# Optimization experiments

Hardware: AMD Instinct MI355X
Metric: run time of the kernel (lower is better)

The kernel has to match this reference:

```python
import jax, jax.numpy as jnp
import numpy as np

N, F, H, C, E, L = 100000, 512, 64, 40, 1600000, 6


def setup_inputs() -> dict:
    key = jax.random.key(0)
    ks = jax.random.split(key, 2 * L + 4)
    x = jax.random.normal(ks[0], (N, F), dtype=jnp.float32)
    edge_index = jax.random.randint(ks[1], (2, E), 0, N, dtype=jnp.int32)
    inp = {"x": x, "edge_index": edge_index}
    in_dims = [F + H * i for i in range(L)]  # 512, 576, ..., 832 (dense concat)
    for i in range(L):
        inp[f"W{i}"] = jax.random.normal(ks[2 + i], (in_dims[i], H), dtype=jnp.float32) / np.sqrt(in_dims[i]).astype(np.float32)
        inp[f"b{i}"] = jnp.zeros((H,), dtype=jnp.float32)
    jk_dim = in_dims[-1] + H  # 896 = num_features + 6*H
    inp["Wlin"] = jax.random.normal(ks[2 + L], (jk_dim, C), dtype=jnp.float32) / np.sqrt(jk_dim).astype(np.float32)
    inp["blin"] = jnp.zeros((C,), dtype=jnp.float32)
    return inp


def _gcn_norm(edge_index, num_nodes, dtype):
    # Add self loops, compute symmetric normalization deg^-1/2 * deg^-1/2
    loop = jnp.arange(num_nodes, dtype=edge_index.dtype)
    row = jnp.concatenate([edge_index[0], loop])  # source
    col = jnp.concatenate([edge_index[1], loop])  # target
    deg = jax.ops.segment_sum(jnp.ones_like(col, dtype=dtype), col, num_segments=num_nodes)
    dinv = jnp.where(deg > 0, jax.lax.rsqrt(jnp.maximum(deg, 1.0)), 0.0)
    norm = dinv[row] * dinv[col]  # [E + N]
    return row, col, norm


def reference(x, edge_index, W0, b0, W1, b1, W2, b2, W3, b3, W4, b4, W5, b5, Wlin, blin):
    Ws = [W0, W1, W2, W3, W4, W5]
    bs = [b0, b1, b2, b3, b4, b5]
    n = x.shape[0]
    row, col, norm = _gcn_norm(edge_index, n, x.dtype)

    xs = [x]
    for W, b in zip(Ws, bs):
        inp = jnp.concatenate(xs, axis=1)          # dense (DenseNet-style) concat
        lin = inp @ W                               # [n, H] transform before propagate
        msg = lin[row] * norm[:, None]              # gather + edge weight
        agg = jax.ops.segment_sum(msg, col, num_segments=n)  # scatter-add aggregate
        h = jax.nn.relu(agg + b)                    # GCNConv bias, then ReLU (dropout = eval mode)
        xs.append(h)

    hcat = jnp.concatenate(xs, axis=1)              # JumpingKnowledge('cat')
    logits = hcat @ Wlin + blin
    return jax.nn.log_softmax(logits, axis=1)
```

## Files before the change

kernel.cpp:

```cpp
#include <hip/hip_runtime.h>
#include <hip/hip_bf16.h>

#define HH 64
#define XDIM 896
#define FF 512
#define LL 6
#define CC 40
#define CBSZ 512
#define SLACK 10240
#define NSEG 13

typedef __bf16 bf16x8 __attribute__((ext_vector_type(8)));
typedef float f32x4 __attribute__((ext_vector_type(4)));

__device__ __forceinline__ unsigned short f2bf(float f){
  union{float f; unsigned int u;} v; v.f=f; unsigned int u=v.u;
  return (unsigned short)((u + 0x7fffu + ((u>>16)&1u))>>16);
}
__device__ __forceinline__ float bf2f(unsigned short u){
  union{unsigned int u; float f;} v; v.u = ((unsigned int)u)<<16; return v.f;
}
__device__ __forceinline__ float u2f(unsigned u){
  union{unsigned u; float f;} v; v.u=u; return v.f;
}

#define GLD16(gsrc, ldsdst) \
  __builtin_amdgcn_global_load_lds((const __attribute__((address_space(1))) unsigned int*)(gsrc), \
                                   (__attribute__((address_space(3))) unsigned int*)(ldsdst), 16, 0, 0)

struct PrepP {
  const float* x; const int* ei;
  unsigned short* X; unsigned short* lin;
  int* bcur; unsigned* tmp;
  const float* W[NSEG]; unsigned short* dst[NSEG];
  int nt[NSEG], nc[NSEG], tst[NSEG], tbs[NSEG], kbase[NSEG];
  int off[NSEG+1];
  int N, E, CH, NB, WB;
};

__global__ void __launch_bounds__(256) k_prep(PrepP P){
  __shared__ int hist[256];
  __shared__ int run[256];
  int t=threadIdx.x, b=blockIdx.x;
  if (b < 256){
    int E=P.E;
    int lo=b*P.CH, hi=lo+P.CH; if (hi>E) hi=E;
    for (int i=t;i<P.NB;i+=256) hist[i]=0;
    __syncthreads();
    for (int i=lo+t;i<hi;i+=256) atomicAdd(&hist[P.ei[E+i]>>9], 1);
    __syncthreads();
    for (int i=t;i<P.NB;i+=256) run[i]=i*SLACK+atomicAdd(&P.bcur[i], hist[i]);
    __syncthreads();
    for (int i=lo+t;i<hi;i+=256){
      int r=P.ei[i], c=P.ei[E+i];
      int pos=atomicAdd(&run[c>>9],1);
      P.tmp[pos]=((unsigned)r<<9)|(unsigned)(c&(CBSZ-1));
    }
  } else if (b < 256+P.WB){
    int idx=(b-256)*256+t;
    if (idx < P.off[NSEG]){
      int seg=0;
      while (idx>=P.off[seg+1]) ++seg;
      int li=idx-P.off[seg];
      int j=li&7, ln=(li>>3)&63, rem2=li>>9;
      int ntile=P.nt[seg], ncols=P.nc[seg];
      int nt_=rem2%ntile, kb=rem2/ntile;
      int k=P.kbase[seg]+kb*32+(ln>>4)*8+j;
      int c=nt_*16+(ln&15);
      float v=(c<ncols)? P.W[seg][(size_t)k*ncols+c] : 0.f;
      int di = ((kb*P.tst[seg] + P.tbs[seg] + nt_)*64 + ln)*8 + j;
      P.dst[seg][di]=f2bf(v);
    }
  } else {
    int i=(b-256-P.WB)*256+t;
    if (i<32) ((unsigned*)(P.lin+(size_t)P.N*64))[i]=0u;
    int total=P.N*(FF/4);
    if (i<total){
      int row=i/(FF/4), c4=(i%(FF/4))*4;
      float4 v=*(const float4*)(P.x+(size_t)row*FF+c4);
      ushort4 o; o.x=f2bf(v.x); o.y=f2bf(v.y); o.z=f2bf(v.z); o.w=f2bf(v.w);
      *(ushort4*)(P.X+(size_t)row*XDIM+c4)=o;
    }
  }
}

__global__ void __launch_bounds__(1024) k_build(const unsigned* __restrict__ tmp,
                                                const int* __restrict__ bcur,
                                                int* __restrict__ offsS, int* __restrict__ offsE,
                                                float* __restrict__ dinv,
                                                int* __restrict__ esrc, int N){
  __shared__ int cnt[CBSZ];
  __shared__ int run[CBSZ];
  int t=threadIdx.x, b=blockIdx.x;
  int n0=b*CBSZ;
  int nloc=N-n0; if (nloc>CBSZ) nloc=CBSZ;
  int wbase=b*SLACK;
  int wend=wbase + bcur[b];
  if (t<CBSZ) cnt[t]=0;
  __syncthreads();
  for (int i=wbase+t; i<wend; i+=1024) atomicAdd(&cnt[tmp[i]&(CBSZ-1u)],1);
  __syncthreads();
  int v = (t<CBSZ)? cnt[t] : 0;
  if (t<CBSZ) run[t]=v;
  __syncthreads();
  for (int o=1;o<CBSZ;o<<=1){
    int xx = (t<CBSZ && t>=o)? run[t-o] : 0;
    __syncthreads();
    if (t<CBSZ) run[t]+=xx;
    __syncthreads();
  }
  if (t<nloc){
    int s = wbase + (run[t]-v);
    offsS[n0+t]=s;
    offsE[n0+t]=s+v;
    dinv[n0+t]=rsqrtf((float)(v+1));
    run[t]=s;
  }
  __syncthreads();
  for (int i=wbase+t; i<wend; i+=1024){
    unsigned vv=tmp[i];
    int pos=atomicAdd(&run[vv&(CBSZ-1u)],1);
    esrc[pos]=(int)(vv>>9);
  }
}

struct GBP {
  const unsigned short* X; const unsigned short* WfBig;
  const float* dinv;
  unsigned short* pl[6];
  float* pF;
  int N;
};

__global__ void __launch_bounds__(256) k_gbig(GBP P){
  __shared__ unsigned short Abuf[2][128*32];
  int t=threadIdx.x, lane=t&63, wv=t>>6;
  int bid = blockIdx.x;
  int cg = bid & 3;
  long rb = (long)(bid>>2)*128;
  int tb = cg*7;
  int arow=lane&15, kgrp=lane>>4;

  int srow0 = wv*32 + (lane>>2);
  int srow1 = srow0 + 16;
  int scb   = 16*((lane&3) ^ (srow0&3));
  long gr0 = rb + srow0; if (gr0 > (long)P.N-1) gr0 = P.N-1;
  long gr1 = rb + srow1; if (gr1 > (long)P.N-1) gr1 = P.N-1;
  const char* gs0 = (const char*)P.X + gr0*(XDIM*2) + scb;
  const char* gs1 = (const char*)P.X + gr1*(XDIM*2) + scb;

  f32x4 acc0[7], acc1[7];
  #pragma unroll
  for (int i=0;i<7;i++){ f32x4 z={0.f,0.f,0.f,0.f}; acc0[i]=z; acc1[i]=z; }

  GLD16(gs0, &Abuf[0][(wv*2+0)*512]);
  GLD16(gs1, &Abuf[0][(wv*2+1)*512]);
  __syncthreads();

  int kofs = 16*(kgrp ^ (arow&3));
  for (int kb=0;kb<16;++kb){
    int cur = kb&1;
    if (kb<15){
      GLD16(gs0 + (kb+1)*64, &Abuf[cur^1][(wv*2+0)*512]);
      GLD16(gs1 + (kb+1)*64, &Abuf[cur^1][(wv*2+1)*512]);
    }
    const unsigned short* bp = P.WfBig + ((size_t)kb*28 + tb)*512 + lane*8;
    bf16x8 bv[7];
    #pragma unroll
    for (int tt=0;tt<7;++tt) bv[tt]=*(const bf16x8*)(bp + (size_t)tt*512);
    int lr0 = wv*32 + arow;
    bf16x8 a0 = *(const bf16x8*)((const char*)&Abuf[cur][0] + lr0*64 + kofs);
    bf16x8 a1 = *(const bf16x8*)((const char*)&Abuf[cur][0] + (lr0+16)*64 + kofs);
    #pragma unroll
    for (int tt=0;tt<7;++tt){
      acc0[tt]=__builtin_amdgcn_mfma_f32_16x16x32_bf16(a0,bv[tt],acc0[tt],0,0,0);
      acc1[tt]=__builtin_amdgcn_mfma_f32_16x16x32_bf16(a1,bv[tt],acc1[tt],0,0,0);
    }
    __syncthreads();
  }

  long row0 = rb + wv*32;
  #pragma unroll
  for (int tt=0;tt<7;++tt){
    int tg = tb+tt;
    if (tg >= 27) continue;
    #pragma unroll
    for (int j=0;j<4;++j){
      long rr=row0+kgrp*4+j;
      long rr1=rr+16;
      if (tg<24){
        int li=tg>>2, tloc=tg&3;
        if (rr<P.N){
          float s = (li==0) ? P.dinv[rr] : 1.f;
          P.pl[li][(size_t)rr*64 + tloc*16 + arow] = f2bf(acc0[tt][j]*s);
        }
        if (rr1<P.N){
          float s = (li==0) ? P.dinv[rr1] : 1.f;
          P.pl[li][(size_t)rr1*64 + tloc*16 + arow] = f2bf(acc1[tt][j]*s);
        }
      } else {
        int c=(tg-24)*16+arow;
        if (c<CC){
          if (rr<P.N)  P.pF[(size_t)rr*CC+c]=acc0[tt][j];
          if (rr1<P.N) P.pF[(size_t)rr1*CC+c]=acc1[tt][j];
        }
      }
    }
  }
}

__global__ void __launch_bounds__(256) k_gemmH(const unsigned short* __restrict__ X,
                                               const unsigned short* __restrict__ WfH,
                                               const unsigned short* __restrict__ part,
                                               const float* __restrict__ dinv,
                                               unsigned short* __restrict__ lin,
                                               int N, int nkb2){
  int lane = threadIdx.x & 63, wid = threadIdx.x >> 6;
  long row0 = (long)blockIdx.x*128 + wid*32;
  int arow = lane & 15, kgrp = lane >> 4;
  long r0 = row0 + arow;      if (r0 > (long)N-1) r0 = N-1;
  long r1 = row0 + 16 + arow; if (r1 > (long)N-1) r1 = N-1;
  const unsigned short* ap0 = X + (size_t)r0*XDIM + FF + kgrp*8;
  const unsigned short* ap1 = X + (size_t)r1*XDIM + FF + kgrp*8;
  const unsigned short* bptr = WfH + lane*8;
  f32x4 acc00={0.f,0.f,0.f,0.f}, acc01=acc00, acc02=acc00, acc03=acc00;
  f32x4 acc10=acc00, acc11=acc00, acc12=acc00, acc13=acc00;
  for (int kb=0; kb<nkb2; ++kb){
    bf16x8 a0 = *(const bf16x8*)(ap0 + (size_t)kb*32);
    bf16x8 a1 = *(const bf16x8*)(ap1 + (size_t)kb*32);
    const unsigned short* bp = bptr + (size_t)kb*2048;
    bf16x8 b0=*(const bf16x8*)bp, b1=*(const bf16x8*)(bp+512),
           b2=*(const bf16x8*)(bp+1024), b3=*(const bf16x8*)(bp+1536);
    acc00=__builtin_amdgcn_mfma_f32_16x16x32_bf16(a0,b0,acc00,0,0,0);
    acc10=__builtin_amdgcn_mfma_f32_16x16x32_bf16(a1,b0,acc10,0,0,0);
    acc01=__builtin_amdgcn_mfma_f32_16x16x32_bf16(a0,b1,acc01,0,0,0);
    acc11=__builtin_amdgcn_mfma_f32_16x16x32_bf16(a1,b1,acc11,0,0,0);
    acc02=__builtin_amdgcn_mfma_f32_16x16x32_bf16(a0,b2,acc02,0,0,0);
    acc12=__builtin_amdgcn_mfma_f32_16x16x32_bf16(a1,b2,acc12,0,0,0);
    acc03=__builtin_amdgcn_mfma_f32_16x16x32_bf16(a0,b3,acc03,0,0,0);
    acc13=__builtin_amdgcn_mfma_f32_16x16x32_bf16(a1,b3,acc13,0,0,0);
  }
  for (int j=0;j<4;++j){
    long rr = row0 + kgrp*4 + j;
    if (rr < N){
      float dv = dinv[rr];
      const unsigned short* pp = part + (size_t)rr*64 + arow;
      unsigned short* lp = lin + (size_t)rr*64 + arow;
      lp[0]  = f2bf((acc00[j]+bf2f(pp[0]))*dv);
      lp[16] = f2bf((acc01[j]+bf2f(pp[16]))*dv);
      lp[32] = f2bf((acc02[j]+bf2f(pp[32]))*dv);
      lp[48] = f2bf((acc03[j]+bf2f(pp[48]))*dv);
    }
    long rr1 = rr + 16;
    if (rr1 < N){
      float dv = dinv[rr1];
      const unsigned short* pp = part + (size_t)rr1*64 + arow;
      unsigned short* lp = lin + (size_t)rr1*64 + arow;
      lp[0]  = f2bf((acc10[j]+bf2f(pp[0]))*dv);
      lp[16] = f2bf((acc11[j]+bf2f(pp[16]))*dv);
      lp[32] = f2bf((acc12[j]+bf2f(pp[32]))*dv);
      lp[48] = f2bf((acc13[j]+bf2f(pp[48]))*dv);
    }
  }
}

__global__ void __launch_bounds__(256) k_agg(const unsigned short* __restrict__ lin,
                                             const int* __restrict__ offsS,
                                             const int* __restrict__ offsE,
                                             const int* __restrict__ esrc,
                                             const float* __restrict__ dinv,
                                             const float* __restrict__ bias,
                                             unsigned short* __restrict__ X,
                                             int colbase, int N){
  int lane = threadIdx.x & 63, wid = threadIdx.x >> 6;
  int n = blockIdx.x*4 + wid;
  if (n >= N) return;
  int sub = lane >> 4;
  int fq  = lane & 15;
  const unsigned short* lq = lin + fq*4;
  float a0=0.f, a1=0.f, a2=0.f, a3=0.f;
  int s = offsS[n], e = offsE[n];
  int base = s;
  for (; base + 32 <= e; base += 32){
    #pragma unroll
    for (int k=0;k<8;++k){
      int sx = esrc[base + 4*k + sub];
      uint2 v = *(const uint2*)(lq + (size_t)sx*64);
      a0 += u2f(v.x<<16); a1 += u2f(v.x&0xffff0000u);
      a2 += u2f(v.y<<16); a3 += u2f(v.y&0xffff0000u);
    }
  }
  if (base < e){
    int rem = e - base;
    if (rem > 16){
      #pragma unroll
      for (int k=0;k<8;++k){
        int idx = 4*k + sub;
        int sx = esrc[base + idx];
        sx = (idx < rem) ? sx : (int)N;
        uint2 v = *(const uint2*)(lq + (size_t)sx*64);
        a0 += u2f(v.x<<16); a1 += u2f(v.x&0xffff0000u);
        a2 += u2f(v.y<<16); a3 += u2f(v.y&0xffff0000u);
      }
    } else {
      #pragma unroll
      for (int k=0;k<4;++k){
        int idx = 4*k + sub;
        int sx = esrc[base + idx];
        sx = (idx < rem) ? sx : (int)N;
        uint2 v = *(const uint2*)(lq + (size_t)sx*64);
        a0 += u2f(v.x<<16); a1 += u2f(v.x&0xffff0000u);
        a2 += u2f(v.y<<16); a3 += u2f(v.y&0xffff0000u);
      }
    }
  }
  a0 += __shfl_xor(a0,16,64); a0 += __shfl_xor(a0,32,64);
  a1 += __shfl_xor(a1,16,64); a1 += __shfl_xor(a1,32,64);
  a2 += __shfl_xor(a2,16,64); a2 += __shfl_xor(a2,32,64);
  a3 += __shfl_xor(a3,16,64); a3 += __shfl_xor(a3,32,64);
  uint2 vs = *(const uint2*)(lq + (size_t)n*64);
  a0 += u2f(vs.x<<16); a1 += u2f(vs.x&0xffff0000u);
  a2 += u2f(vs.y<<16); a3 += u2f(vs.y&0xffff0000u);
  float dv = dinv[n];
  float4 b4 = *(const float4*)(bias + fq*4);
  float h0 = fmaxf(a0*dv + b4.x, 0.f);
  float h1 = fmaxf(a1*dv + b4.y, 0.f);
  float h2 = fmaxf(a2*dv + b4.z, 0.f);
  float h3 = fmaxf(a3*dv + b4.w, 0.f);
  if (sub == 0){
    ushort4 o; o.x=f2bf(h0); o.y=f2bf(h1); o.z=f2bf(h2); o.w=f2bf(h3);
    *(ushort4*)(X + (size_t)n*XDIM + colbase + fq*4) = o;
  }
}

__global__ void __launch_bounds__(256) k_final(const unsigned short* __restrict__ X,
                                               const unsigned short* __restrict__ Wf,
                                               const float* __restrict__ pF,
                                               const float* __restrict__ blin,
                                               float* __restrict__ out, int N){
  int lane=threadIdx.x&63, wid=threadIdx.x>>6;
  long row0=(long)blockIdx.x*64 + wid*16;
  int c0=lane&15, g=lane>>4;
  long r=row0+c0; if (r > (long)N-1) r = N-1;
  const unsigned short* aptr = X + (size_t)r*XDIM + FF + g*8;
  const unsigned short* bptr = Wf + lane*8;
  f32x4 acc0={0.f,0.f,0.f,0.f}, acc1=acc0, acc2=acc0;
  const int nkb = (XDIM-FF)/32;
  for (int kb=0;kb<nkb;++kb){
    bf16x8 a=*(const bf16x8*)(aptr+(size_t)kb*32);
    const unsigned short* bp = bptr + (size_t)kb*1536;
    bf16x8 b0=*(const bf16x8*)bp, b1=*(const bf16x8*)(bp+512), b2=*(const bf16x8*)(bp+1024);
    acc0=__builtin_amdgcn_mfma_f32_16x16x32_bf16(a,b0,acc0,0,0,0);
    acc1=__builtin_amdgcn_mfma_f32_16x16x32_bf16(a,b1,acc1,0,0,0);
    acc2=__builtin_amdgcn_mfma_f32_16x16x32_bf16(a,b2,acc2,0,0,0);
  }
  float bl0 = blin[c0], bl1 = blin[16+c0];
  bool v2ok = (c0 < 8);
  float bl2 = v2ok ? blin[32+c0] : 0.f;
  for (int j=0;j<4;++j){
    long rr = row0 + g*4 + j;
    long rrc = rr < N ? rr : (long)N-1;
    const float* pp = pF + (size_t)rrc*CC;
    float v0 = acc0[j]+bl0+pp[c0], v1 = acc1[j]+bl1+pp[16+c0];
    float v2 = v2ok ? (acc2[j]+bl2+pp[32+c0]) : -1e30f;
    float m = fmaxf(fmaxf(v0,v1),v2);
    m = fmaxf(m, __shfl_xor(m,1,64));
    m = fmaxf(m, __shfl_xor(m,2,64));
    m = fmaxf(m, __shfl_xor(m,4,64));
    m = fmaxf(m, __shfl_xor(m,8,64));
    float sEx = expf(v0-m)+expf(v1-m)+(v2ok?expf(v2-m):0.f);
    sEx += __shfl_xor(sEx,1,64);
    sEx += __shfl_xor(sEx,2,64);
    sEx += __shfl_xor(sEx,4,64);
    sEx += __shfl_xor(sEx,8,64);
    float lse = m + logf(sEx);
    if (rr < N){
      out[(size_t)rr*CC + c0]      = v0 - lse;
      out[(size_t)rr*CC + 16 + c0] = v1 - lse;
      if (v2ok) out[(size_t)rr*CC + 32 + c0] = v2 - lse;
    }
  }
}

extern "C" void kernel_launch(void* const* d_in, const int* in_sizes, int n_in,
                              void* d_out, int out_size, void* d_ws, size_t ws_size,
                              hipStream_t stream){
  const float* x = (const float*)d_in[0];
  const int* ei = (const int*)d_in[1];
  const float* Wl[LL]; const float* bl[LL];
  for (int i=0;i<LL;i++){ Wl[i]=(const float*)d_in[2+2*i]; bl[i]=(const float*)d_in[3+2*i]; }
  const float* Wlin = (const float*)d_in[2+2*LL];
  const float* blin = (const float*)d_in[3+2*LL];
  float* out = (float*)d_out;
  const int N = in_sizes[0]/FF;
  const int E = in_sizes[1]/2;
  const int NB = (N+CBSZ-1)/CBSZ;

  char* p = (char*)d_ws;
  auto alloc = [&](size_t bb)->char*{ char* r=p; p += (bb+255)&~(size_t)255; return r; };
  unsigned short* X   = (unsigned short*)alloc((size_t)N*XDIM*2);
  unsigned short* lin = (unsigned short*)alloc((size_t)(N+1)*64*2);
  unsigned* tmp = (unsigned*)lin;
  unsigned short* WfBig  = (unsigned short*)alloc((size_t)16*28*512*2);
  unsigned short* WfH[LL];
  for (int i=1;i<LL;i++) WfH[i]=(unsigned short*)alloc((size_t)(2*i)*4*512*2);
  unsigned short* WfLinH = (unsigned short*)alloc((size_t)12*3*512*2);
  unsigned short* part[LL];
  for (int i=1;i<LL;i++) part[i]=(unsigned short*)alloc((size_t)N*64*2);
  float* pF    = (float*)alloc((size_t)N*CC*4);
  float* dinv  = (float*)alloc((size_t)N*4);
  int* offsS   = (int*)alloc((size_t)N*4);
  int* offsE   = (int*)alloc((size_t)N*4);
  int* bcur    = (int*)alloc((size_t)NB*4);
  int* esrc    = (int*)alloc(((size_t)NB*SLACK+64)*4);

  PrepP P;
  P.x=x; P.ei=ei; P.X=X; P.lin=lin; P.bcur=bcur; P.tmp=tmp;
  int off=0, sg=0;
  for (int i=0;i<LL;i++){
    P.W[sg]=Wl[i]; P.dst[sg]=WfBig; P.nt[sg]=4; P.nc[sg]=HH;
    P.tst[sg]=28; P.tbs[sg]=4*i; P.kbase[sg]=0;
    P.off[sg]=off; off += 16*4*512; ++sg;
  }
  P.W[sg]=Wlin; P.dst[sg]=WfBig; P.nt[sg]=3; P.nc[sg]=CC;
  P.tst[sg]=28; P.tbs[sg]=24; P.kbase[sg]=0;
  P.off[sg]=off; off += 16*3*512; ++sg;
  for (int i=1;i<LL;i++){
    P.W[sg]=Wl[i]; P.dst[sg]=WfH[i]; P.nt[sg]=4; P.nc[sg]=HH;
    P.tst[sg]=4; P.tbs[sg]=0; P.kbase[sg]=FF;
    P.off[sg]=off; off += (2*i)*4*512; ++sg;
  }
  P.W[sg]=Wlin; P.dst[sg]=WfLinH; P.nt[sg]=3; P.nc[sg]=CC;
  P.tst[sg]=3; P.tbs[sg]=0; P.kbase[sg]=FF;
  P.off[sg]=off; off += 12*3*512; ++sg;
  P.off[sg]=off;
  P.N=N; P.E=E; P.CH=(E+255)/256; P.NB=NB; P.WB=(off+255)/256;
  int XB=(N*(FF/4)+255)/256;

  hipMemsetAsync(bcur, 0, (size_t)NB*4, stream);
  k_prep <<<256 + P.WB + XB, 256, 0, stream>>>(P);
  k_build<<<NB, 1024, 0, stream>>>(tmp, bcur, offsS, offsE, dinv, esrc, N);

  GBP G;
  G.X=X; G.WfBig=WfBig; G.dinv=dinv;
  G.pl[0]=lin;
  for (int i=1;i<LL;i++) G.pl[i]=part[i];
  G.pF=pF; G.N=N;
  int rbks = (N+127)/128;
  k_gbig<<<rbks*4, 256, 0, stream>>>(G);

  int gb = (N+127)/128;
  int ab = (N+3)/4;
  for (int i=0;i<LL;i++){
    if (i>0) k_gemmH<<<gb,256,0,stream>>>(X, WfH[i], part[i], dinv, lin, N, 2*i);
    k_agg<<<ab,256,0,stream>>>(lin, offsS, offsE, esrc, dinv, bl[i], X, FF+HH*i, N);
  }
  k_final<<<(N+63)/64,256,0,stream>>>(X, WfLinH, pF, blin, out, N);
}
```

Measured before the change: 594.7 us.

## Split lin into four 16-column planes and aggregate one plane per block

```diff
diff --git a/kernel.cpp b/kernel.cpp
--- a/kernel.cpp
+++ b/kernel.cpp
@@ -73,7 +73,6 @@
     }
   } else {
     int i=(b-256-P.WB)*256+t;
-    if (i<32) ((unsigned*)(P.lin+(size_t)P.N*64))[i]=0u;
     int total=P.N*(FF/4);
     if (i<total){
       int row=i/(FF/4), c4=(i%(FF/4))*4;
@@ -136,6 +135,10 @@
   __shared__ unsigned short Abuf[2][128*32];
   int t=threadIdx.x, lane=t&63, wv=t>>6;
   int bid = blockIdx.x;
+  if (bid==0 && t<32){
+    int c=t>>3, d=t&7;
+    ((unsigned*)(P.pl[0] + ((size_t)c*(P.N+1) + P.N)*16))[d] = 0u;
+  }
   int cg = bid & 3;
   long rb = (long)(bid>>2)*128;
   int tb = cg*7;
@@ -190,13 +193,12 @@
       long rr1=rr+16;
       if (tg<24){
         int li=tg>>2, tloc=tg&3;
-        if (rr<P.N){
-          float s = (li==0) ? P.dinv[rr] : 1.f;
-          P.pl[li][(size_t)rr*64 + tloc*16 + arow] = f2bf(acc0[tt][j]*s);
-        }
-        if (rr1<P.N){
-          float s = (li==0) ? P.dinv[rr1] : 1.f;
-          P.pl[li][(size_t)rr1*64 + tloc*16 + arow] = f2bf(acc1[tt][j]*s);
+        if (li==0){
+          if (rr<P.N)  P.pl[0][((size_t)tloc*(P.N+1)+rr )*16 + arow] = f2bf(acc0[tt][j]*P.dinv[rr]);
+          if (rr1<P.N) P.pl[0][((size_t)tloc*(P.N+1)+rr1)*16 + arow] = f2bf(acc1[tt][j]*P.dinv[rr1]);
+        } else {
+          if (rr<P.N)  P.pl[li][(size_t)rr *64 + tloc*16 + arow] = f2bf(acc0[tt][j]);
+          if (rr1<P.N) P.pl[li][(size_t)rr1*64 + tloc*16 + arow] = f2bf(acc1[tt][j]);
         }
       } else {
         int c=(tg-24)*16+arow;
@@ -245,91 +247,83 @@
     if (rr < N){
       float dv = dinv[rr];
       const unsigned short* pp = part + (size_t)rr*64 + arow;
-      unsigned short* lp = lin + (size_t)rr*64 + arow;
-      lp[0]  = f2bf((acc00[j]+bf2f(pp[0]))*dv);
-      lp[16] = f2bf((acc01[j]+bf2f(pp[16]))*dv);
-      lp[32] = f2bf((acc02[j]+bf2f(pp[32]))*dv);
-      lp[48] = f2bf((acc03[j]+bf2f(pp[48]))*dv);
+      lin[((size_t)0*(N+1)+rr)*16 + arow] = f2bf((acc00[j]+bf2f(pp[0]))*dv);
+      lin[((size_t)1*(N+1)+rr)*16 + arow] = f2bf((acc01[j]+bf2f(pp[16]))*dv);
+      lin[((size_t)2*(N+1)+rr)*16 + arow] = f2bf((acc02[j]+bf2f(pp[32]))*dv);
+      lin[((size_t)3*(N+1)+rr)*16 + arow] = f2bf((acc03[j]+bf2f(pp[48]))*dv);
     }
     long rr1 = rr + 16;
     if (rr1 < N){
       float dv = dinv[rr1];
       const unsigned short* pp = part + (size_t)rr1*64 + arow;
-      unsigned short* lp = lin + (size_t)rr1*64 + arow;
-      lp[0]  = f2bf((acc10[j]+bf2f(pp[0]))*dv);
-      lp[16] = f2bf((acc11[j]+bf2f(pp[16]))*dv);
-      lp[32] = f2bf((acc12[j]+bf2f(pp[32]))*dv);
-      lp[48] = f2bf((acc13[j]+bf2f(pp[48]))*dv);
-    }
-  }
-}
-
-__global__ void __launch_bounds__(256) k_agg(const unsigned short* __restrict__ lin,
+      lin[((size_t)0*(N+1)+rr1)*16 + arow] = f2bf((acc10[j]+bf2f(pp[0]))*dv);
+      lin[((size_t)1*(N+1)+rr1)*16 + arow] = f2bf((acc11[j]+bf2f(pp[16]))*dv);
+      lin[((size_t)2*(N+1)+rr1)*16 + arow] = f2bf((acc12[j]+bf2f(pp[32]))*dv);
+      lin[((size_t)3*(N+1)+rr1)*16 + arow] = f2bf((acc13[j]+bf2f(pp[48]))*dv);
+    }
+  }
+}
+
+__global__ void __launch_bounds__(256) k_agg(const unsigned short* __restrict__ lin4,
                                              const int* __restrict__ offsS,
                                              const int* __restrict__ offsE,
                                              const int* __restrict__ esrc,
                                              const float* __restrict__ dinv,
                                              const float* __restrict__ bias,
                                              unsigned short* __restrict__ X,
-                                             int colbase, int N){
+                                             int colbase, int N, int nb4){
   int lane = threadIdx.x & 63, wid = threadIdx.x >> 6;
-  int n = blockIdx.x*4 + wid;
+  int chunk = blockIdx.x / nb4;
+  int nbid  = blockIdx.x - chunk*nb4;
+  int n = nbid*4 + wid;
   if (n >= N) return;
-  int sub = lane >> 4;
-  int fq  = lane & 15;
-  const unsigned short* lq = lin + fq*4;
-  float a0=0.f, a1=0.f, a2=0.f, a3=0.f;
+  int sub = lane >> 2;
+  int fj  = lane & 3;
+  const unsigned short* lq = lin4 + (size_t)chunk*(N+1)*16 + fj*4;
+  float a0=0.f,a1=0.f,a2=0.f,a3=0.f;
   int s = offsS[n], e = offsE[n];
   int base = s;
   for (; base + 32 <= e; base += 32){
-    #pragma unroll
-    for (int k=0;k<8;++k){
-      int sx = esrc[base + 4*k + sub];
-      uint2 v = *(const uint2*)(lq + (size_t)sx*64);
-      a0 += u2f(v.x<<16); a1 += u2f(v.x&0xffff0000u);
-      a2 += u2f(v.y<<16); a3 += u2f(v.y&0xffff0000u);
-    }
+    int sx0 = esrc[base + sub];
+    int sx1 = esrc[base + 16 + sub];
+    uint2 v0 = *(const uint2*)(lq + (size_t)sx0*16);
+    uint2 v1 = *(const uint2*)(lq + (size_t)sx1*16);
+    a0 += u2f(v0.x<<16); a1 += u2f(v0.x&0xffff0000u);
+    a2 += u2f(v0.y<<16); a3 += u2f(v0.y&0xffff0000u);
+    a0 += u2f(v1.x<<16); a1 += u2f(v1.x&0xffff0000u);
+    a2 += u2f(v1.y<<16); a3 += u2f(v1.y&0xffff0000u);
   }
   if (base < e){
     int rem = e - base;
+    int sx0 = esrc[base + sub];
+    sx0 = (sub < rem) ? sx0 : (int)N;
+    uint2 v0 = *(const uint2*)(lq + (size_t)sx0*16);
+    a0 += u2f(v0.x<<16); a1 += u2f(v0.x&0xffff0000u);
+    a2 += u2f(v0.y<<16); a3 += u2f(v0.y&0xffff0000u);
     if (rem > 16){
-      #pragma unroll
-      for (int k=0;k<8;++k){
-        int idx = 4*k + sub;
-        int sx = esrc[base + idx];
-        sx = (idx < rem) ? sx : (int)N;
-        uint2 v = *(const uint2*)(lq + (size_t)sx*64);
-        a0 += u2f(v.x<<16); a1 += u2f(v.x&0xffff0000u);
-        a2 += u2f(v.y<<16); a3 += u2f(v.y&0xffff0000u);
-      }
-    } else {
-      #pragma unroll
-      for (int k=0;k<4;++k){
-        int idx = 4*k + sub;
-        int sx = esrc[base + idx];
-        sx = (idx < rem) ? sx : (int)N;
-        uint2 v = *(const uint2*)(lq + (size_t)sx*64);
-        a0 += u2f(v.x<<16); a1 += u2f(v.x&0xffff0000u);
-        a2 += u2f(v.y<<16); a3 += u2f(v.y&0xffff0000u);
-      }
-    }
-  }
-  a0 += __shfl_xor(a0,16,64); a0 += __shfl_xor(a0,32,64);
-  a1 += __shfl_xor(a1,16,64); a1 += __shfl_xor(a1,32,64);
-  a2 += __shfl_xor(a2,16,64); a2 += __shfl_xor(a2,32,64);
-  a3 += __shfl_xor(a3,16,64); a3 += __shfl_xor(a3,32,64);
-  uint2 vs = *(const uint2*)(lq + (size_t)n*64);
+      int sx1 = esrc[base + 16 + sub];
+      sx1 = (16 + sub < rem) ? sx1 : (int)N;
+      uint2 v1 = *(const uint2*)(lq + (size_t)sx1*16);
+      a0 += u2f(v1.x<<16); a1 += u2f(v1.x&0xffff0000u);
+      a2 += u2f(v1.y<<16); a3 += u2f(v1.y&0xffff0000u);
+    }
+  }
+  a0 += __shfl_xor(a0,4,64); a0 += __shfl_xor(a0,8,64); a0 += __shfl_xor(a0,16,64); a0 += __shfl_xor(a0,32,64);
+  a1 += __shfl_xor(a1,4,64); a1 += __shfl_xor(a1,8,64); a1 += __shfl_xor(a1,16,64); a1 += __shfl_xor(a1,32,64);
+  a2 += __shfl_xor(a2,4,64); a2 += __shfl_xor(a2,8,64); a2 += __shfl_xor(a2,16,64); a2 += __shfl_xor(a2,32,64);
+  a3 += __shfl_xor(a3,4,64); a3 += __shfl_xor(a3,8,64); a3 += __shfl_xor(a3,16,64); a3 += __shfl_xor(a3,32,64);
+  uint2 vs = *(const uint2*)(lq + (size_t)n*16);
   a0 += u2f(vs.x<<16); a1 += u2f(vs.x&0xffff0000u);
   a2 += u2f(vs.y<<16); a3 += u2f(vs.y&0xffff0000u);
   float dv = dinv[n];
-  float4 b4 = *(const float4*)(bias + fq*4);
+  float4 b4 = *(const float4*)(bias + chunk*16 + fj*4);
   float h0 = fmaxf(a0*dv + b4.x, 0.f);
   float h1 = fmaxf(a1*dv + b4.y, 0.f);
   float h2 = fmaxf(a2*dv + b4.z, 0.f);
   float h3 = fmaxf(a3*dv + b4.w, 0.f);
   if (sub == 0){
     ushort4 o; o.x=f2bf(h0); o.y=f2bf(h1); o.z=f2bf(h2); o.w=f2bf(h3);
-    *(ushort4*)(X + (size_t)n*XDIM + colbase + fq*4) = o;
+    *(ushort4*)(X + (size_t)n*XDIM + colbase + chunk*16 + fj*4) = o;
   }
 }
 
@@ -399,7 +393,7 @@
   char* p = (char*)d_ws;
   auto alloc = [&](size_t bb)->char*{ char* r=p; p += (bb+255)&~(size_t)255; return r; };
   unsigned short* X   = (unsigned short*)alloc((size_t)N*XDIM*2);
-  unsigned short* lin = (unsigned short*)alloc((size_t)(N+1)*64*2);
+  unsigned short* lin = (unsigned short*)alloc((size_t)4*(N+1)*16*2);
   unsigned* tmp = (unsigned*)lin;
   unsigned short* WfBig  = (unsigned short*)alloc((size_t)16*28*512*2);
   unsigned short* WfH[LL];
@@ -453,7 +447,7 @@
   int ab = (N+3)/4;
   for (int i=0;i<LL;i++){
     if (i>0) k_gemmH<<<gb,256,0,stream>>>(X, WfH[i], part[i], dinv, lin, N, 2*i);
-    k_agg<<<ab,256,0,stream>>>(lin, offsS, offsE, esrc, dinv, bl[i], X, FF+HH*i, N);
+    k_agg<<<4*ab,256,0,stream>>>(lin, offsS, offsE, esrc, dinv, bl[i], X, FF+HH*i, N, ab);
   }
   k_final<<<(N+63)/64,256,0,stream>>>(X, WfLinH, pF, blin, out, N);
 }
```

Result: slower. 1.089 ms (+83.0%).

## Remap k_gbig blocks to 32 rows with waves splitting output column tiles

Applied to the files above, without the earlier changes.

```diff
diff --git a/kernel.cpp b/kernel.cpp
--- a/kernel.cpp
+++ b/kernel.cpp
@@ -133,44 +133,37 @@
 };
 
 __global__ void __launch_bounds__(256) k_gbig(GBP P){
-  __shared__ unsigned short Abuf[2][128*32];
+  __shared__ unsigned short Abuf[2][1024];
   int t=threadIdx.x, lane=t&63, wv=t>>6;
-  int bid = blockIdx.x;
-  int cg = bid & 3;
-  long rb = (long)(bid>>2)*128;
-  int tb = cg*7;
+  int tb = wv*7;
+  long rb = (long)blockIdx.x*32;
   int arow=lane&15, kgrp=lane>>4;
 
-  int srow0 = wv*32 + (lane>>2);
-  int srow1 = srow0 + 16;
-  int scb   = 16*((lane&3) ^ (srow0&3));
-  long gr0 = rb + srow0; if (gr0 > (long)P.N-1) gr0 = P.N-1;
-  long gr1 = rb + srow1; if (gr1 > (long)P.N-1) gr1 = P.N-1;
-  const char* gs0 = (const char*)P.X + gr0*(XDIM*2) + scb;
-  const char* gs1 = (const char*)P.X + gr1*(XDIM*2) + scb;
+  const char* gs = nullptr;
+  if (wv < 2){
+    int srow = wv*16 + (lane>>2);
+    int scb  = 16*((lane&3) ^ (srow&3));
+    long gr = rb + srow; if (gr > (long)P.N-1) gr = P.N-1;
+    gs = (const char*)P.X + gr*(XDIM*2) + scb;
+  }
 
   f32x4 acc0[7], acc1[7];
   #pragma unroll
   for (int i=0;i<7;i++){ f32x4 z={0.f,0.f,0.f,0.f}; acc0[i]=z; acc1[i]=z; }
 
-  GLD16(gs0, &Abuf[0][(wv*2+0)*512]);
-  GLD16(gs1, &Abuf[0][(wv*2+1)*512]);
+  if (wv < 2) GLD16(gs, &Abuf[0][wv*512]);
   __syncthreads();
 
-  int kofs = 16*(kgrp ^ (arow&3));
+  int kof0 = 16*(kgrp ^ (arow&3));
   for (int kb=0;kb<16;++kb){
     int cur = kb&1;
-    if (kb<15){
-      GLD16(gs0 + (kb+1)*64, &Abuf[cur^1][(wv*2+0)*512]);
-      GLD16(gs1 + (kb+1)*64, &Abuf[cur^1][(wv*2+1)*512]);
-    }
+    if (kb<15 && wv<2) GLD16(gs + (kb+1)*64, &Abuf[cur^1][wv*512]);
     const unsigned short* bp = P.WfBig + ((size_t)kb*28 + tb)*512 + lane*8;
     bf16x8 bv[7];
     #pragma unroll
     for (int tt=0;tt<7;++tt) bv[tt]=*(const bf16x8*)(bp + (size_t)tt*512);
-    int lr0 = wv*32 + arow;
-    bf16x8 a0 = *(const bf16x8*)((const char*)&Abuf[cur][0] + lr0*64 + kofs);
-    bf16x8 a1 = *(const bf16x8*)((const char*)&Abuf[cur][0] + (lr0+16)*64 + kofs);
+    bf16x8 a0 = *(const bf16x8*)((const char*)&Abuf[cur][0] + arow*64 + kof0);
+    bf16x8 a1 = *(const bf16x8*)((const char*)&Abuf[cur][0] + (arow+16)*64 + kof0);
     #pragma unroll
     for (int tt=0;tt<7;++tt){
       acc0[tt]=__builtin_amdgcn_mfma_f32_16x16x32_bf16(a0,bv[tt],acc0[tt],0,0,0);
@@ -179,7 +172,7 @@
     __syncthreads();
   }
 
-  long row0 = rb + wv*32;
+  long row0 = rb;
   #pragma unroll
   for (int tt=0;tt<7;++tt){
     int tg = tb+tt;
@@ -446,8 +439,7 @@
   G.pl[0]=lin;
   for (int i=1;i<LL;i++) G.pl[i]=part[i];
   G.pF=pF; G.N=N;
-  int rbks = (N+127)/128;
-  k_gbig<<<rbks*4, 256, 0, stream>>>(G);
+  k_gbig<<<(N+31)/32, 256, 0, stream>>>(G);
 
   int gb = (N+127)/128;
   int ab = (N+3)/4;
```

New measurement: 584.6 us. No clear change (-1.7%).
